# Performance work log

Hardware: AMD Instinct MI355X
Metric: run time of the kernel (lower is better)

Reference implementation:

```python
import jax, jax.numpy as jnp
import numpy as np

B, T, E, H = 2, 2048, 1024, 16
D = E // H  # head_dim = 64


def setup_inputs() -> dict:
    key = jax.random.key(0)
    kx, kq, kk, kv, ko = jax.random.split(key, 5)
    x = jax.random.normal(kx, (B, T, E), dtype=jnp.float32)
    # nn.Parameter(torch.randn(...)) -> standard normal params
    Wq = jax.random.normal(kq, (H, E, D), dtype=jnp.float32)
    Wk = jax.random.normal(kk, (H, E, D), dtype=jnp.float32)
    Wv = jax.random.normal(kv, (H, E, D), dtype=jnp.float32)
    # nn.Linear(E, E, bias=False): weight [out, in], y = a @ Wo.T
    Wo = jax.random.normal(ko, (E, E), dtype=jnp.float32) * (1.0 / np.sqrt(E))
    # boolean mask: True positions are filled with -inf (causal: strict upper tri)
    mask = jnp.triu(jnp.ones((T, T), dtype=bool), k=1)
    return {"x": x, "mask": mask, "Wq": Wq, "Wk": Wk, "Wv": Wv, "Wo": Wo}


def reference(x, mask, Wq, Wk, Wv, Wo):
    # x: [b, t, e]; Wq/Wk/Wv: [h, e, i]
    q = jnp.einsum('hei,bte->hbti', Wq, x)
    k = jnp.einsum('hei,bte->hbti', Wk, x)
    v = jnp.einsum('hei,bte->hbti', Wv, x)
    # NOTE: original scales by sqrt(seq_len) (x.shape[1]), not sqrt(head_dim)
    scale = x.shape[1] ** 0.5
    fit = jnp.einsum('hbti,hbTi->hbtT', q, k) / scale  # [h, b, t, T]
    fit = jnp.where(mask, -jnp.inf, fit)
    p = jax.nn.softmax(fit, axis=-1)
    att = jnp.einsum('hbtT,hbTi->hbti', p, v)          # [h, b, t, i]
    # rearrange 'h b t i -> b t (h i)'
    b, t = att.shape[1], att.shape[2]
    att = jnp.transpose(att, (1, 2, 0, 3)).reshape(b, t, -1)
    return att @ Wo.T
```

## Files before the change

kernel.cpp:

```cpp
#include <hip/hip_runtime.h>
#include <hip/hip_fp8.h>
#include <stdint.h>

constexpr float INV_SCALE = 0.022097086912079608f;
constexpr float LOG2E = 1.4426950408889634f;
constexpr float QSC = INV_SCALE * LOG2E;

typedef __attribute__((ext_vector_type(8))) short bfrag;
typedef __attribute__((ext_vector_type(4))) float facc;
typedef __attribute__((ext_vector_type(4))) unsigned short us4;

#define MFMA(a, b, c) __builtin_amdgcn_mfma_f32_16x16x32_bf16((a), (b), (c), 0, 0, 0)
#define EXP2(x) __builtin_amdgcn_exp2f(x)

__device__ __forceinline__ unsigned short f2bh(float f) {
    union { float f; unsigned int u; } cv; cv.f = f;
    unsigned int u = cv.u;
    u += 0x7FFFu + ((u >> 16) & 1u);
    return (unsigned short)(u >> 16);
}
__device__ __forceinline__ float bh2f(unsigned short h) {
    union { unsigned int u; float f; } cv; cv.u = ((unsigned int)h) << 16;
    return cv.f;
}
__device__ __forceinline__ void gl_lds16(const unsigned short* g, unsigned short* lds) {
    __builtin_amdgcn_global_load_lds(
        (const __attribute__((address_space(1))) unsigned int*)g,
        (__attribute__((address_space(3))) unsigned int*)lds, 16, 0, 0);
}
__device__ __forceinline__ bfrag f8frag(uint2 raw) {
    union { uint2 u; unsigned char b[8]; } cv; cv.u = raw;
    bfrag r;
    #pragma unroll
    for (int j = 0; j < 8; ++j) {
        const __hip_fp8_e4m3* t = reinterpret_cast<const __hip_fp8_e4m3*>(&cv.b[j]);
        r[j] = (short)f2bh((float)(*t) * 0.00390625f);
    }
    return r;
}

__global__ __launch_bounds__(256) void x_split(const float* __restrict__ x,
                                               unsigned short* __restrict__ xh,
                                               unsigned short* __restrict__ xl) {
    int idx = blockIdx.x * 256 + threadIdx.x;
    facc v = *(const facc*)&x[(size_t)idx * 4];
    us4 hv, lv;
    #pragma unroll
    for (int j = 0; j < 4; ++j) {
        unsigned short hb = f2bh(v[j]);
        hv[j] = hb;
        lv[j] = f2bh(v[j] - bh2f(hb));
    }
    *(us4*)&xh[(size_t)idx * 4] = hv;
    *(us4*)&xl[(size_t)idx * 4] = lv;
}

__global__ __launch_bounds__(256) void prep_w(
    const float* __restrict__ Wq, const float* __restrict__ Wk, const float* __restrict__ Wv,
    unsigned short* __restrict__ WqTh, unsigned short* __restrict__ WqTl,
    unsigned short* __restrict__ WkTh, unsigned short* __restrict__ WkTl,
    unsigned short* __restrict__ WvT)
{
    __shared__ float tile[64][65];
    const int tid = threadIdx.x;
    const int et = blockIdx.x, h = blockIdx.y, m = blockIdx.z;
    const float* W = (m == 0) ? Wq : (m == 1) ? Wk : Wv;
    #pragma unroll
    for (int rep = 0; rep < 4; ++rep) {
        int idx = rep * 256 + tid;
        int e = idx >> 4, i4 = (idx & 15) * 4;
        facc v = *(const facc*)&W[(size_t)h * 65536 + (size_t)(et * 64 + e) * 64 + i4];
        tile[e][i4] = v.x; tile[e][i4 + 1] = v.y; tile[e][i4 + 2] = v.z; tile[e][i4 + 3] = v.w;
    }
    __syncthreads();
    unsigned short* Oh = (m == 0) ? WqTh : (m == 1) ? WkTh : WvT;
    unsigned short* Ol = (m == 0) ? WqTl : WkTl;
    #pragma unroll
    for (int rep = 0; rep < 4; ++rep) {
        int idx = rep * 256 + tid;
        int i = idx >> 4, e4 = (idx & 15) * 4;
        us4 hv, lv;
        #pragma unroll
        for (int j = 0; j < 4; ++j) {
            float f = tile[e4 + j][i];
            unsigned short hb = f2bh(f);
            hv[j] = hb;
            lv[j] = f2bh(f - bh2f(hb));
        }
        size_t o = (size_t)(h * 64 + i) * 1024 + et * 64 + e4;
        *(us4*)&Oh[o] = hv;
        if (m < 2) *(us4*)&Ol[o] = lv;
    }
}

__global__ __launch_bounds__(256) void wo_conv(const float* __restrict__ Wo,
                                               unsigned short* __restrict__ WoB) {
    int idx = blockIdx.x * 256 + threadIdx.x;
    facc v = *(const facc*)&Wo[(size_t)idx * 4];
    us4 o;
    #pragma unroll
    for (int j = 0; j < 4; ++j) o[j] = f2bh(v[j]);
    *(us4*)&WoB[(size_t)idx * 4] = o;
}

__global__ __launch_bounds__(512, 2) void qkv_fused(
    const unsigned short* __restrict__ xh, const unsigned short* __restrict__ xl,
    const unsigned short* __restrict__ WqTh, const unsigned short* __restrict__ WqTl,
    const unsigned short* __restrict__ WkTh, const unsigned short* __restrict__ WkTl,
    const unsigned short* __restrict__ WvT,
    unsigned short* __restrict__ qh, unsigned char* __restrict__ ql8,
    unsigned short* __restrict__ kh, unsigned short* __restrict__ kl,
    unsigned short* __restrict__ vT)
{
    extern __shared__ unsigned short sm[];
    unsigned short* Ab = sm;
    unsigned short* Qb = sm + 16384;
    unsigned short* Kb = sm + 32768;
    unsigned short* Vb = sm + 49152;
    const int tid = threadIdx.x;
    const int w = tid >> 6, l = tid & 63;
    const int wm = w >> 2, wn = w & 3;
    const int ct = blockIdx.x, rt = blockIdx.y;

    const int lc = (l & 7) ^ (l >> 3);
    const int krel = (lc & 3) * 8;
    const unsigned short* Axp = (lc < 4) ? xh : xl;
    const unsigned short* Qp  = (lc < 4) ? WqTh : WqTl;
    const unsigned short* Kp  = (lc < 4) ? WkTh : WkTl;

    facc accq[4][2], acck[4][2], accv[4][2];
    #pragma unroll
    for (int m = 0; m < 4; ++m)
        #pragma unroll
        for (int n = 0; n < 2; ++n) {
            accq[m][n] = (facc)(0.0f); acck[m][n] = (facc)(0.0f); accv[m][n] = (facc)(0.0f);
        }

    auto stageAB = [&](int buf, int e0) {
        #pragma unroll
        for (int i = 0; i < 2; ++i) {
            int slice = w * 2 + i;
            int row = slice * 8 + (l >> 3);
            size_t sa = (size_t)(rt * 128 + row) * 1024 + e0 + krel;
            size_t sb = (size_t)(ct * 128 + row) * 1024 + e0 + krel;
            gl_lds16(&Axp[sa], &Ab[buf * 8192 + slice * 512]);
            gl_lds16(&Qp[sb],  &Qb[buf * 8192 + slice * 512]);
            gl_lds16(&Kp[sb],  &Kb[buf * 8192 + slice * 512]);
        }
    };

    stageAB(0, 0);
    #pragma unroll
    for (int i = 0; i < 2; ++i) {
        int slice = w * 2 + i;
        int row = slice * 8 + (l >> 3);
        gl_lds16(&WvT[(size_t)(ct * 128 + row) * 1024 + lc * 8], &Vb[slice * 512]);
    }
    asm volatile("s_waitcnt vmcnt(0)" ::: "memory");
    __builtin_amdgcn_s_barrier();

    for (int t = 0; t < 32; ++t) {
        __builtin_amdgcn_s_barrier();
        __builtin_amdgcn_sched_barrier(0);
        if (t < 31) stageAB((t + 1) & 1, (t + 1) * 32);
        {
            int wv = (t >> 1) + 1;
            if (wv < 16) {
                int slice = w + (t & 1) * 8;
                int row = slice * 8 + (l >> 3);
                gl_lds16(&WvT[(size_t)(ct * 128 + row) * 1024 + wv * 64 + lc * 8],
                         &Vb[(wv & 1) * 8192 + slice * 512]);
            }
        }
        __builtin_amdgcn_sched_barrier(0);
        if (t < 30)       asm volatile("s_waitcnt vmcnt(7)" ::: "memory");
        else if (t == 30) asm volatile("s_waitcnt vmcnt(6)" ::: "memory");
        else              asm volatile("s_waitcnt vmcnt(0)" ::: "memory");
        __builtin_amdgcn_sched_barrier(0);
        __builtin_amdgcn_s_barrier();
        __builtin_amdgcn_sched_barrier(0);

        const unsigned short* Ac = &Ab[(t & 1) * 8192];
        const unsigned short* Qc = &Qb[(t & 1) * 8192];
        const unsigned short* Kc = &Kb[(t & 1) * 8192];
        const unsigned short* Vc = &Vb[((t >> 1) & 1) * 8192];
        const int ca = (l >> 4) ^ (l & 7);
        const int cb = ca ^ 4;
        const int cv = ca ^ ((t & 1) << 2);

        bfrag afh[4], afl[4];
        #pragma unroll
        for (int m = 0; m < 4; ++m) {
            int row = wm * 64 + m * 16 + (l & 15);
            afh[m] = *(const bfrag*)&Ac[row * 64 + ca * 8];
            afl[m] = *(const bfrag*)&Ac[row * 64 + cb * 8];
        }
        #pragma unroll
        for (int n = 0; n < 2; ++n) {
            int nr = wn * 32 + n * 16 + (l & 15);
            bfrag bv = *(const bfrag*)&Vc[nr * 64 + cv * 8];
            #pragma unroll
            for (int m = 0; m < 4; ++m) accv[m][n] = MFMA(afh[m], bv, accv[m][n]);
        }
        #pragma unroll
        for (int n = 0; n < 2; ++n) {
            int nr = wn * 32 + n * 16 + (l & 15);
            bfrag bh = *(const bfrag*)&Qc[nr * 64 + ca * 8];
            bfrag bl = *(const bfrag*)&Qc[nr * 64 + cb * 8];
            #pragma unroll
            for (int m = 0; m < 4; ++m) {
                accq[m][n] = MFMA(afh[m], bh, accq[m][n]);
                accq[m][n] = MFMA(afh[m], bl, accq[m][n]);
                accq[m][n] = MFMA(afl[m], bh, accq[m][n]);
            }
        }
        #pragma unroll
        for (int n = 0; n < 2; ++n) {
            int nr = wn * 32 + n * 16 + (l & 15);
            bfrag bh = *(const bfrag*)&Kc[nr * 64 + ca * 8];
            bfrag bl = *(const bfrag*)&Kc[nr * 64 + cb * 8];
            #pragma unroll
            for (int m = 0; m < 4; ++m) {
                acck[m][n] = MFMA(afh[m], bh, acck[m][n]);
                acck[m][n] = MFMA(afh[m], bl, acck[m][n]);
                acck[m][n] = MFMA(afl[m], bh, acck[m][n]);
            }
        }
    }

    #pragma unroll
    for (int m = 0; m < 4; ++m)
        #pragma unroll
        for (int r = 0; r < 4; ++r) {
            int row = rt * 128 + wm * 64 + m * 16 + (l >> 4) * 4 + r;
            #pragma unroll
            for (int n = 0; n < 2; ++n) {
                int col = ct * 128 + wn * 32 + n * 16 + (l & 15);
                float fq = accq[m][n][r] * QSC;
                unsigned short hb = f2bh(fq);
                qh[(size_t)row * 1024 + col] = hb;
                __hip_fp8_e4m3 e((fq - bh2f(hb)) * 256.0f);
                ql8[(size_t)row * 1024 + col] = *reinterpret_cast<unsigned char*>(&e);
                float fk = acck[m][n][r];
                unsigned short kb = f2bh(fk);
                kh[(size_t)row * 1024 + col] = kb;
                kl[(size_t)row * 1024 + col] = f2bh(fk - bh2f(kb));
            }
        }
    #pragma unroll
    for (int m = 0; m < 4; ++m) {
        int t0g = rt * 128 + wm * 64 + m * 16 + (l >> 4) * 4;
        int b_ = t0g >> 11, t0 = t0g & 2047;
        #pragma unroll
        for (int n = 0; n < 2; ++n) {
            int col = ct * 128 + wn * 32 + n * 16 + (l & 15);
            int h_ = col >> 6, d = col & 63;
            us4 pk;
            #pragma unroll
            for (int r = 0; r < 4; ++r) pk[r] = f2bh(accv[m][n][r]);
            *(us4*)&vT[((size_t)((h_ * 2 + b_) * 64 + d)) * 2048 + t0] = pk;
        }
    }
}

__device__ __forceinline__ void stage_kv(
    const unsigned short* __restrict__ kh, const unsigned short* __restrict__ kl,
    const unsigned short* __restrict__ vT,
    unsigned short* Khb, unsigned short* Klb, unsigned short* Vtb,
    int w, int l, int b, int h, int kt)
{
    #pragma unroll
    for (int i = 0; i < 2; ++i) {
        int pbase = (w * 2 + i) * 1024;
        int p = pbase + l * 16;
        int row = p >> 7, slot = (p >> 4) & 7;
        int chunk = slot ^ (row & 7);
        size_t srcK = (size_t)(b * 2048 + kt * 64 + row) * 1024 + h * 64 + chunk * 8;
        size_t srcV = ((size_t)(h * 2 + b) * 64 + row) * 2048 + (size_t)kt * 64 + chunk * 8;
        gl_lds16(&kh[srcK], &Khb[pbase >> 1]);
        gl_lds16(&kl[srcK], &Klb[pbase >> 1]);
        gl_lds16(&vT[srcV], &Vtb[pbase >> 1]);
    }
}

__device__ __forceinline__ void attn_step(
    const unsigned short* Khb, const unsigned short* Klb, const unsigned short* Vtb,
    unsigned short* Pl, const bfrag* qfh, const bfrag* qfl,
    facc* O, float* mrow, float* lrow, int w, int l, bool diag)
{
    facc S[4];
    #pragma unroll
    for (int f = 0; f < 4; ++f) S[f] = (facc)(0.0f);
    #pragma unroll
    for (int s = 0; s < 2; ++s) {
        #pragma unroll
        for (int f = 0; f < 4; ++f) {
            int key = f * 16 + (l & 15);
            int ch = (s * 4 + (l >> 4)) ^ (key & 7);
            bfrag kbh = *(const bfrag*)&Khb[key * 64 + ch * 8];
            bfrag kbl = *(const bfrag*)&Klb[key * 64 + ch * 8];
            S[f] = MFMA(qfh[s], kbh, S[f]);
            S[f] = MFMA(qfh[s], kbl, S[f]);
            S[f] = MFMA(qfl[s], kbh, S[f]);
        }
    }
    if (diag) {
        #pragma unroll
        for (int f = 0; f < 4; ++f) {
            int keyl = f * 16 + (l & 15);
            #pragma unroll
            for (int r = 0; r < 4; ++r) {
                int qls = w * 16 + (l >> 4) * 4 + r;
                if (keyl > qls) S[f][r] = -1e30f;
            }
        }
    }
    #pragma unroll
    for (int r = 0; r < 4; ++r) {
        float mx = fmaxf(fmaxf(S[0][r], S[1][r]), fmaxf(S[2][r], S[3][r]));
        mx = fmaxf(mx, __shfl_xor(mx, 1));
        mx = fmaxf(mx, __shfl_xor(mx, 2));
        mx = fmaxf(mx, __shfl_xor(mx, 4));
        mx = fmaxf(mx, __shfl_xor(mx, 8));
        float mn = fmaxf(mrow[r], mx);
        float fac = EXP2(mrow[r] - mn);
        mrow[r] = mn;
        float rs = 0.0f;
        #pragma unroll
        for (int f = 0; f < 4; ++f) { S[f][r] = EXP2(S[f][r] - mn); rs += S[f][r]; }
        rs += __shfl_xor(rs, 1); rs += __shfl_xor(rs, 2);
        rs += __shfl_xor(rs, 4); rs += __shfl_xor(rs, 8);
        lrow[r] = lrow[r] * fac + rs;
        O[0][r] *= fac; O[1][r] *= fac; O[2][r] *= fac; O[3][r] *= fac;
    }
    #pragma unroll
    for (int f = 0; f < 4; ++f) {
        int key = f * 16 + (l & 15);
        #pragma unroll
        for (int r = 0; r < 4; ++r) {
            int qr = w * 16 + (l >> 4) * 4 + r;
            Pl[qr * 64 + (((key >> 3) ^ (qr & 7)) * 8) + (key & 7)] = f2bh(S[f][r]);
        }
    }
    #pragma unroll
    for (int s = 0; s < 2; ++s) {
        int qa = w * 16 + (l & 15);
        int cha = (s * 4 + (l >> 4)) ^ (qa & 7);
        bfrag pa = *(const bfrag*)&Pl[qa * 64 + cha * 8];
        #pragma unroll
        for (int f = 0; f < 4; ++f) {
            int d = f * 16 + (l & 15);
            int chv = (s * 4 + (l >> 4)) ^ (d & 7);
            bfrag vb = *(const bfrag*)&Vtb[d * 64 + chv * 8];
            O[f] = MFMA(pa, vb, O[f]);
        }
    }
}

__global__ __launch_bounds__(256, 2) void attn_mfma(
    const unsigned short* __restrict__ qh, const unsigned char* __restrict__ ql8,
    const unsigned short* __restrict__ kh, const unsigned short* __restrict__ kl,
    const unsigned short* __restrict__ vT, unsigned short* __restrict__ att)
{
    __shared__ unsigned short Kh[2][64 * 64], Kl[2][64 * 64], Vt[2][64 * 64], Pl[64 * 64];
    const int tid = threadIdx.x, w = tid >> 6, l = tid & 63;
    const int dd = blockIdx.y * 16 + blockIdx.x;
    const int xcd = dd & 7, sl = dd >> 3;
    const int hb = xcd * 4 + (sl >> 4);
    const int bx = sl & 15;
    const int qtA = 31 - bx, qtB = bx;
    const int h = hb >> 1, b = hb & 1;

    bfrag qfhA[2], qflA[2], qfhB[2], qflB[2];
    {
        const int qrowA = qtA * 64 + w * 16 + (l & 15);
        const size_t qoffA = (size_t)(b * 2048 + qrowA) * 1024 + h * 64 + (l >> 4) * 8;
        qfhA[0] = *(const bfrag*)&qh[qoffA];
        qfhA[1] = *(const bfrag*)&qh[qoffA + 32];
        qflA[0] = f8frag(*(const uint2*)&ql8[qoffA]);
        qflA[1] = f8frag(*(const uint2*)&ql8[qoffA + 32]);
        const int qrowB = qtB * 64 + w * 16 + (l & 15);
        const size_t qoffB = (size_t)(b * 2048 + qrowB) * 1024 + h * 64 + (l >> 4) * 8;
        qfhB[0] = *(const bfrag*)&qh[qoffB];
        qfhB[1] = *(const bfrag*)&qh[qoffB + 32];
        qflB[0] = f8frag(*(const uint2*)&ql8[qoffB]);
        qflB[1] = f8frag(*(const uint2*)&ql8[qoffB + 32]);
    }

    facc OA[4], OB[4];
    float mA[4], lA[4], mB[4], lB[4];
    #pragma unroll
    for (int f = 0; f < 4; ++f) { OA[f] = (facc)(0.0f); OB[f] = (facc)(0.0f); }
    #pragma unroll
    for (int r = 0; r < 4; ++r) { mA[r] = -1e30f; lA[r] = 0.0f; mB[r] = -1e30f; lB[r] = 0.0f; }

    stage_kv(kh, kl, vT, Kh[0], Kl[0], Vt[0], w, l, b, h, 0);
    int cur = 0;
    for (int kt = 0; kt <= qtA; ++kt) {
        __syncthreads();
        if (kt < qtA)
            stage_kv(kh, kl, vT, Kh[cur ^ 1], Kl[cur ^ 1], Vt[cur ^ 1], w, l, b, h, kt + 1);
        __builtin_amdgcn_sched_barrier(0);
        __builtin_amdgcn_s_barrier();
        __builtin_amdgcn_sched_barrier(0);
        attn_step(Kh[cur], Kl[cur], Vt[cur], Pl, qfhA, qflA, OA, mA, lA, w, l, kt == qtA);
        if (kt <= qtB)
            attn_step(Kh[cur], Kl[cur], Vt[cur], Pl, qfhB, qflB, OB, mB, lB, w, l, kt == qtB);
        cur ^= 1;
    }

    #pragma unroll
    for (int f = 0; f < 4; ++f) {
        int d = h * 64 + f * 16 + (l & 15);
        #pragma unroll
        for (int r = 0; r < 4; ++r) {
            int tA = qtA * 64 + w * 16 + (l >> 4) * 4 + r;
            att[(size_t)(b * 2048 + tA) * 1024 + d] = f2bh(OA[f][r] / lA[r]);
            int tB = qtB * 64 + w * 16 + (l >> 4) * 4 + r;
            att[(size_t)(b * 2048 + tB) * 1024 + d] = f2bh(OB[f][r] / lB[r]);
        }
    }
}

__global__ __launch_bounds__(256, 2) void outproj(
    const unsigned short* __restrict__ att, const unsigned short* __restrict__ WoB,
    float* __restrict__ out)
{
    __shared__ unsigned short Ab[2][128 * 64], Bb[2][128 * 64];
    const int tid = threadIdx.x, w = tid >> 6, l = tid & 63;
    const int wm = w >> 1, wn = w & 1;
    const int rt = blockIdx.x, ct = blockIdx.y;

    const int lc = (l & 7) ^ (l >> 3);
    facc acc[4][4];
    #pragma unroll
    for (int i = 0; i < 4; ++i)
        #pragma unroll
        for (int j = 0; j < 4; ++j) acc[i][j] = (facc)(0.0f);

    auto stage = [&](int buf, int e0) {
        #pragma unroll
        for (int i = 0; i < 4; ++i) {
            int slice = w * 4 + i;
            int row = slice * 8 + (l >> 3);
            gl_lds16(&att[(size_t)(rt * 128 + row) * 1024 + e0 + lc * 8], &Ab[buf][slice * 512]);
            gl_lds16(&WoB[(size_t)(ct * 128 + row) * 1024 + e0 + lc * 8], &Bb[buf][slice * 512]);
        }
    };

    stage(0, 0);
    int cur = 0;
    for (int t = 0; t < 16; ++t) {
        __syncthreads();
        if (t < 15) stage(cur ^ 1, (t + 1) * 64);
        __builtin_amdgcn_sched_barrier(0);
        __builtin_amdgcn_s_barrier();
        __builtin_amdgcn_sched_barrier(0);
        #pragma unroll
        for (int s = 0; s < 2; ++s) {
            const int slot = (s * 4 + (l >> 4)) ^ (l & 7);
            bfrag af[4], bf_[4];
            #pragma unroll
            for (int m = 0; m < 4; ++m)
                af[m] = *(const bfrag*)&Ab[cur][(wm * 64 + m * 16 + (l & 15)) * 64 + slot * 8];
            #pragma unroll
            for (int n = 0; n < 4; ++n)
                bf_[n] = *(const bfrag*)&Bb[cur][(wn * 64 + n * 16 + (l & 15)) * 64 + slot * 8];
            #pragma unroll
            for (int m = 0; m < 4; ++m)
                #pragma unroll
                for (int n = 0; n < 4; ++n)
                    acc[m][n] = MFMA(af[m], bf_[n], acc[m][n]);
        }
        cur ^= 1;
    }
    #pragma unroll
    for (int m = 0; m < 4; ++m)
        #pragma unroll
        for (int r = 0; r < 4; ++r) {
            int row = rt * 128 + wm * 64 + m * 16 + (l >> 4) * 4 + r;
            #pragma unroll
            for (int n = 0; n < 4; ++n) {
                int col = ct * 128 + wn * 64 + n * 16 + (l & 15);
                out[(size_t)row * 1024 + col] = acc[m][n][r];
            }
        }
}

extern "C" void kernel_launch(void* const* d_in, const int* in_sizes, int n_in,
                              void* d_out, int out_size, void* d_ws, size_t ws_size,
                              hipStream_t stream) {
    const float* x  = (const float*)d_in[0];
    const float* Wq = (const float*)d_in[2];
    const float* Wk = (const float*)d_in[3];
    const float* Wv = (const float*)d_in[4];
    const float* Wo = (const float*)d_in[5];

    uint8_t* wsb = (uint8_t*)d_ws;
    const size_t MB = 1024 * 1024;
    unsigned short* WqTh = (unsigned short*)(wsb + 0 * MB);
    unsigned short* WqTl = (unsigned short*)(wsb + 2 * MB);
    unsigned short* WkTh = (unsigned short*)(wsb + 4 * MB);
    unsigned short* WkTl = (unsigned short*)(wsb + 6 * MB);
    unsigned short* WvT  = (unsigned short*)(wsb + 8 * MB);
    unsigned short* qh   = (unsigned short*)(wsb + 10 * MB);
    unsigned char*  ql8  = (unsigned char*)(wsb + 18 * MB);
    unsigned short* kh   = (unsigned short*)(wsb + 22 * MB);
    unsigned short* kl   = (unsigned short*)(wsb + 30 * MB);
    unsigned short* vT   = (unsigned short*)(wsb + 38 * MB);
    unsigned short* att  = (unsigned short*)(wsb + 46 * MB);
    unsigned short* xh   = (unsigned short*)(wsb + 46 * MB);
    unsigned short* WoB  = (unsigned short*)(wsb + 54 * MB);
    unsigned short* xl   = (unsigned short*)(wsb + 56 * MB);

    hipFuncSetAttribute((const void*)qkv_fused,
                        hipFuncAttributeMaxDynamicSharedMemorySize, 131072);

    x_split<<<dim3(4096), 256, 0, stream>>>(x, xh, xl);
    prep_w<<<dim3(16, 16, 3), 256, 0, stream>>>(Wq, Wk, Wv, WqTh, WqTl, WkTh, WkTl, WvT);
    wo_conv<<<dim3(1024), 256, 0, stream>>>(Wo, WoB);
    qkv_fused<<<dim3(8, 32), 512, 131072, stream>>>(xh, xl, WqTh, WqTl, WkTh, WkTl, WvT,
                                                    qh, ql8, kh, kl, vT);
    attn_mfma<<<dim3(16, 32), 256, 0, stream>>>(qh, ql8, kh, kl, vT, att);
    outproj<<<dim3(32, 8), 256, 0, stream>>>(att, WoB, (float*)d_out);
}
```

Baseline: 172.9 us.

## Interleave paired query tiles in attention loop, add lazy rescale, merge prep kernels

The attention loop now runs both query tiles' QK MFMAs together on each K fragment load and shares the V fragment loads in PV, using separate P buffers in dynamic shared memory. Softmax skips the running-max rescale of O and l unless some row's max grows by more than 8 (log2 units), which removes exps and multiplies on most tiles. The x split and Wo conversion kernels are merged into one launch. In exchange there are more live registers, which can lower occupancy, and the lazy rescale lets unnormalized exponentials reach up to 2^8 in bf16 P.

```diff
diff --git a/kernel.cpp b/kernel.cpp
--- a/kernel.cpp
+++ b/kernel.cpp
@@ -39,20 +39,31 @@
     return r;
 }
 
-__global__ __launch_bounds__(256) void x_split(const float* __restrict__ x,
+__global__ __launch_bounds__(256) void prep_xw(const float* __restrict__ x,
+                                               const float* __restrict__ Wo,
                                                unsigned short* __restrict__ xh,
-                                               unsigned short* __restrict__ xl) {
-    int idx = blockIdx.x * 256 + threadIdx.x;
-    facc v = *(const facc*)&x[(size_t)idx * 4];
-    us4 hv, lv;
-    #pragma unroll
-    for (int j = 0; j < 4; ++j) {
-        unsigned short hb = f2bh(v[j]);
-        hv[j] = hb;
-        lv[j] = f2bh(v[j] - bh2f(hb));
-    }
-    *(us4*)&xh[(size_t)idx * 4] = hv;
-    *(us4*)&xl[(size_t)idx * 4] = lv;
+                                               unsigned short* __restrict__ xl,
+                                               unsigned short* __restrict__ WoB) {
+    if (blockIdx.x < 1024) {
+        int idx = blockIdx.x * 256 + threadIdx.x;
+        facc v = *(const facc*)&Wo[(size_t)idx * 4];
+        us4 o;
+        #pragma unroll
+        for (int j = 0; j < 4; ++j) o[j] = f2bh(v[j]);
+        *(us4*)&WoB[(size_t)idx * 4] = o;
+    } else {
+        int idx = (blockIdx.x - 1024) * 256 + threadIdx.x;
+        facc v = *(const facc*)&x[(size_t)idx * 4];
+        us4 hv, lv;
+        #pragma unroll
+        for (int j = 0; j < 4; ++j) {
+            unsigned short hb = f2bh(v[j]);
+            hv[j] = hb;
+            lv[j] = f2bh(v[j] - bh2f(hb));
+        }
+        *(us4*)&xh[(size_t)idx * 4] = hv;
+        *(us4*)&xl[(size_t)idx * 4] = lv;
+    }
 }
 
 __global__ __launch_bounds__(256) void prep_w(
@@ -91,16 +102,6 @@
         *(us4*)&Oh[o] = hv;
         if (m < 2) *(us4*)&Ol[o] = lv;
     }
-}
-
-__global__ __launch_bounds__(256) void wo_conv(const float* __restrict__ Wo,
-                                               unsigned short* __restrict__ WoB) {
-    int idx = blockIdx.x * 256 + threadIdx.x;
-    facc v = *(const facc*)&Wo[(size_t)idx * 4];
-    us4 o;
-    #pragma unroll
-    for (int j = 0; j < 4; ++j) o[j] = f2bh(v[j]);
-    *(us4*)&WoB[(size_t)idx * 4] = o;
 }
 
 __global__ __launch_bounds__(512, 2) void qkv_fused(
@@ -283,55 +284,52 @@
     }
 }
 
-__device__ __forceinline__ void attn_step(
-    const unsigned short* Khb, const unsigned short* Klb, const unsigned short* Vtb,
-    unsigned short* Pl, const bfrag* qfh, const bfrag* qfl,
-    facc* O, float* mrow, float* lrow, int w, int l, bool diag)
+__device__ __forceinline__ void causal_mask(facc* S, int w, int l) {
+    #pragma unroll
+    for (int f = 0; f < 4; ++f) {
+        int keyl = f * 16 + (l & 15);
+        #pragma unroll
+        for (int r = 0; r < 4; ++r) {
+            int qls = w * 16 + (l >> 4) * 4 + r;
+            if (keyl > qls) S[f][r] = -1e30f;
+        }
+    }
+}
+
+__device__ __forceinline__ void softmax_pw(
+    facc* S, float* mrow, float* lrow, facc* O,
+    unsigned short* Pl, int w, int l)
 {
-    facc S[4];
-    #pragma unroll
-    for (int f = 0; f < 4; ++f) S[f] = (facc)(0.0f);
-    #pragma unroll
-    for (int s = 0; s < 2; ++s) {
-        #pragma unroll
-        for (int f = 0; f < 4; ++f) {
-            int key = f * 16 + (l & 15);
-            int ch = (s * 4 + (l >> 4)) ^ (key & 7);
-            bfrag kbh = *(const bfrag*)&Khb[key * 64 + ch * 8];
-            bfrag kbl = *(const bfrag*)&Klb[key * 64 + ch * 8];
-            S[f] = MFMA(qfh[s], kbh, S[f]);
-            S[f] = MFMA(qfh[s], kbl, S[f]);
-            S[f] = MFMA(qfl[s], kbh, S[f]);
-        }
-    }
-    if (diag) {
-        #pragma unroll
-        for (int f = 0; f < 4; ++f) {
-            int keyl = f * 16 + (l & 15);
-            #pragma unroll
-            for (int r = 0; r < 4; ++r) {
-                int qls = w * 16 + (l >> 4) * 4 + r;
-                if (keyl > qls) S[f][r] = -1e30f;
-            }
-        }
-    }
+    float mx[4];
+    float dmax = -3.0e38f;
     #pragma unroll
     for (int r = 0; r < 4; ++r) {
-        float mx = fmaxf(fmaxf(S[0][r], S[1][r]), fmaxf(S[2][r], S[3][r]));
-        mx = fmaxf(mx, __shfl_xor(mx, 1));
-        mx = fmaxf(mx, __shfl_xor(mx, 2));
-        mx = fmaxf(mx, __shfl_xor(mx, 4));
-        mx = fmaxf(mx, __shfl_xor(mx, 8));
-        float mn = fmaxf(mrow[r], mx);
-        float fac = EXP2(mrow[r] - mn);
-        mrow[r] = mn;
+        float m0 = fmaxf(fmaxf(S[0][r], S[1][r]), fmaxf(S[2][r], S[3][r]));
+        m0 = fmaxf(m0, __shfl_xor(m0, 1));
+        m0 = fmaxf(m0, __shfl_xor(m0, 2));
+        m0 = fmaxf(m0, __shfl_xor(m0, 4));
+        m0 = fmaxf(m0, __shfl_xor(m0, 8));
+        mx[r] = m0;
+        dmax = fmaxf(dmax, m0 - mrow[r]);
+    }
+    if (!__all(dmax <= 8.0f)) {
+        #pragma unroll
+        for (int r = 0; r < 4; ++r) {
+            float mn = fmaxf(mrow[r], mx[r]);
+            float fac = EXP2(mrow[r] - mn);
+            mrow[r] = mn;
+            lrow[r] *= fac;
+            O[0][r] *= fac; O[1][r] *= fac; O[2][r] *= fac; O[3][r] *= fac;
+        }
+    }
+    #pragma unroll
+    for (int r = 0; r < 4; ++r) {
         float rs = 0.0f;
         #pragma unroll
-        for (int f = 0; f < 4; ++f) { S[f][r] = EXP2(S[f][r] - mn); rs += S[f][r]; }
+        for (int f = 0; f < 4; ++f) { S[f][r] = EXP2(S[f][r] - mrow[r]); rs += S[f][r]; }
         rs += __shfl_xor(rs, 1); rs += __shfl_xor(rs, 2);
         rs += __shfl_xor(rs, 4); rs += __shfl_xor(rs, 8);
-        lrow[r] = lrow[r] * fac + rs;
-        O[0][r] *= fac; O[1][r] *= fac; O[2][r] *= fac; O[3][r] *= fac;
+        lrow[r] += rs;
     }
     #pragma unroll
     for (int f = 0; f < 4; ++f) {
@@ -340,19 +338,6 @@
         for (int r = 0; r < 4; ++r) {
             int qr = w * 16 + (l >> 4) * 4 + r;
             Pl[qr * 64 + (((key >> 3) ^ (qr & 7)) * 8) + (key & 7)] = f2bh(S[f][r]);
-        }
-    }
-    #pragma unroll
-    for (int s = 0; s < 2; ++s) {
-        int qa = w * 16 + (l & 15);
-        int cha = (s * 4 + (l >> 4)) ^ (qa & 7);
-        bfrag pa = *(const bfrag*)&Pl[qa * 64 + cha * 8];
-        #pragma unroll
-        for (int f = 0; f < 4; ++f) {
-            int d = f * 16 + (l & 15);
-            int chv = (s * 4 + (l >> 4)) ^ (d & 7);
-            bfrag vb = *(const bfrag*)&Vtb[d * 64 + chv * 8];
-            O[f] = MFMA(pa, vb, O[f]);
         }
     }
 }
@@ -362,7 +347,12 @@
     const unsigned short* __restrict__ kh, const unsigned short* __restrict__ kl,
     const unsigned short* __restrict__ vT, unsigned short* __restrict__ att)
 {
-    __shared__ unsigned short Kh[2][64 * 64], Kl[2][64 * 64], Vt[2][64 * 64], Pl[64 * 64];
+    extern __shared__ unsigned short smA[];
+    unsigned short* Kh = smA;
+    unsigned short* Kl = smA + 8192;
+    unsigned short* Vt = smA + 16384;
+    unsigned short* PlA = smA + 24576;
+    unsigned short* PlB = smA + 28672;
     const int tid = threadIdx.x, w = tid >> 6, l = tid & 63;
     const int dd = blockIdx.y * 16 + blockIdx.x;
     const int xcd = dd & 7, sl = dd >> 3;
@@ -394,19 +384,92 @@
     #pragma unroll
     for (int r = 0; r < 4; ++r) { mA[r] = -1e30f; lA[r] = 0.0f; mB[r] = -1e30f; lB[r] = 0.0f; }
 
-    stage_kv(kh, kl, vT, Kh[0], Kl[0], Vt[0], w, l, b, h, 0);
-    int cur = 0;
+    stage_kv(kh, kl, vT, Kh, Kl, Vt, w, l, b, h, 0);
     for (int kt = 0; kt <= qtA; ++kt) {
+        const int cur = kt & 1;
         __syncthreads();
         if (kt < qtA)
-            stage_kv(kh, kl, vT, Kh[cur ^ 1], Kl[cur ^ 1], Vt[cur ^ 1], w, l, b, h, kt + 1);
+            stage_kv(kh, kl, vT, &Kh[(cur ^ 1) * 4096], &Kl[(cur ^ 1) * 4096],
+                     &Vt[(cur ^ 1) * 4096], w, l, b, h, kt + 1);
         __builtin_amdgcn_sched_barrier(0);
         __builtin_amdgcn_s_barrier();
         __builtin_amdgcn_sched_barrier(0);
-        attn_step(Kh[cur], Kl[cur], Vt[cur], Pl, qfhA, qflA, OA, mA, lA, w, l, kt == qtA);
-        if (kt <= qtB)
-            attn_step(Kh[cur], Kl[cur], Vt[cur], Pl, qfhB, qflB, OB, mB, lB, w, l, kt == qtB);
-        cur ^= 1;
+
+        const unsigned short* Khc = &Kh[cur * 4096];
+        const unsigned short* Klc = &Kl[cur * 4096];
+        const unsigned short* Vtc = &Vt[cur * 4096];
+
+        if (kt <= qtB) {
+            facc SA[4], SB[4];
+            #pragma unroll
+            for (int f = 0; f < 4; ++f) { SA[f] = (facc)(0.0f); SB[f] = (facc)(0.0f); }
+            #pragma unroll
+            for (int s = 0; s < 2; ++s) {
+                #pragma unroll
+                for (int f = 0; f < 4; ++f) {
+                    int key = f * 16 + (l & 15);
+                    int ch = (s * 4 + (l >> 4)) ^ (key & 7);
+                    bfrag kbh = *(const bfrag*)&Khc[key * 64 + ch * 8];
+                    bfrag kbl = *(const bfrag*)&Klc[key * 64 + ch * 8];
+                    SA[f] = MFMA(qfhA[s], kbh, SA[f]);
+                    SA[f] = MFMA(qfhA[s], kbl, SA[f]);
+                    SA[f] = MFMA(qflA[s], kbh, SA[f]);
+                    SB[f] = MFMA(qfhB[s], kbh, SB[f]);
+                    SB[f] = MFMA(qfhB[s], kbl, SB[f]);
+                    SB[f] = MFMA(qflB[s], kbh, SB[f]);
+                }
+            }
+            if (kt == qtB) causal_mask(SB, w, l);
+            softmax_pw(SA, mA, lA, OA, PlA, w, l);
+            softmax_pw(SB, mB, lB, OB, PlB, w, l);
+            #pragma unroll
+            for (int s = 0; s < 2; ++s) {
+                int qa = w * 16 + (l & 15);
+                int cha = (s * 4 + (l >> 4)) ^ (qa & 7);
+                bfrag paA = *(const bfrag*)&PlA[qa * 64 + cha * 8];
+                bfrag paB = *(const bfrag*)&PlB[qa * 64 + cha * 8];
+                #pragma unroll
+                for (int f = 0; f < 4; ++f) {
+                    int d = f * 16 + (l & 15);
+                    int chv = (s * 4 + (l >> 4)) ^ (d & 7);
+                    bfrag vb = *(const bfrag*)&Vtc[d * 64 + chv * 8];
+                    OA[f] = MFMA(paA, vb, OA[f]);
+                    OB[f] = MFMA(paB, vb, OB[f]);
+                }
+            }
+        } else {
+            facc S[4];
+            #pragma unroll
+            for (int f = 0; f < 4; ++f) S[f] = (facc)(0.0f);
+            #pragma unroll
+            for (int s = 0; s < 2; ++s) {
+                #pragma unroll
+                for (int f = 0; f < 4; ++f) {
+                    int key = f * 16 + (l & 15);
+                    int ch = (s * 4 + (l >> 4)) ^ (key & 7);
+                    bfrag kbh = *(const bfrag*)&Khc[key * 64 + ch * 8];
+                    bfrag kbl = *(const bfrag*)&Klc[key * 64 + ch * 8];
+                    S[f] = MFMA(qfhA[s], kbh, S[f]);
+                    S[f] = MFMA(qfhA[s], kbl, S[f]);
+                    S[f] = MFMA(qflA[s], kbh, S[f]);
+                }
+            }
+            if (kt == qtA) causal_mask(S, w, l);
+            softmax_pw(S, mA, lA, OA, PlA, w, l);
+            #pragma unroll
+            for (int s = 0; s < 2; ++s) {
+                int qa = w * 16 + (l & 15);
+                int cha = (s * 4 + (l >> 4)) ^ (qa & 7);
+                bfrag pa = *(const bfrag*)&PlA[qa * 64 + cha * 8];
+                #pragma unroll
+                for (int f = 0; f < 4; ++f) {
+                    int d = f * 16 + (l & 15);
+                    int chv = (s * 4 + (l >> 4)) ^ (d & 7);
+                    bfrag vb = *(const bfrag*)&Vtc[d * 64 + chv * 8];
+                    OA[f] = MFMA(pa, vb, OA[f]);
+                }
+            }
+        }
     }
 
     #pragma unroll
@@ -515,12 +578,13 @@
 
     hipFuncSetAttribute((const void*)qkv_fused,
                         hipFuncAttributeMaxDynamicSharedMemorySize, 131072);
-
-    x_split<<<dim3(4096), 256, 0, stream>>>(x, xh, xl);
+    hipFuncSetAttribute((const void*)attn_mfma,
+                        hipFuncAttributeMaxDynamicSharedMemorySize, 65536);
+
+    prep_xw<<<dim3(5120), 256, 0, stream>>>(x, Wo, xh, xl, WoB);
     prep_w<<<dim3(16, 16, 3), 256, 0, stream>>>(Wq, Wk, Wv, WqTh, WqTl, WkTh, WkTl, WvT);
-    wo_conv<<<dim3(1024), 256, 0, stream>>>(Wo, WoB);
     qkv_fused<<<dim3(8, 32), 512, 131072, stream>>>(xh, xl, WqTh, WqTl, WkTh, WkTl, WvT,
                                                     qh, ql8, kh, kl, vT);
-    attn_mfma<<<dim3(16, 32), 256, 0, stream>>>(qh, ql8, kh, kl, vT, att);
+    attn_mfma<<<dim3(16, 32), 256, 65536, stream>>>(qh, ql8, kh, kl, vT, att);
     outproj<<<dim3(32, 8), 256, 0, stream>>>(att, WoB, (float*)d_out);
 }
```

Result: slower. 180.5 us (+4.4%).
